# Performance work log

Measured on AMD Instinct MI355X. Metric: run time of the kernel, lower is better.

Reference implementation:

```python
import jax, jax.numpy as jnp
import numpy as np

B, S, H = 1, 2048, 2048
NH = 16
Q_LORA, KV_LORA = 1536, 512
D_NOPE, D_ROPE, D_V = 128, 64, 128
D_QK = D_NOPE + D_ROPE  # 192
EPS = 1e-6
ROPE_BASE = 10000.0


def setup_inputs() -> dict:
    key = jax.random.key(0)
    ks = jax.random.split(key, 8)
    def lin(k, fan_in, fan_out):
        # nn.Linear default init, stored as [in, out] for x @ W
        bound = 1.0 / np.sqrt(fan_in)
        return jax.random.uniform(k, (fan_in, fan_out), jnp.float32, -bound, bound)
    return {
        "hidden_states": jax.random.normal(ks[0], (B, S, H), jnp.float32),
        "Wqa": lin(ks[1], H, Q_LORA),
        "q_a_ln_w": jnp.ones((Q_LORA,), jnp.float32),
        "Wqb": lin(ks[2], Q_LORA, NH * D_QK),
        "Wkva": lin(ks[3], H, KV_LORA + D_ROPE),
        "kv_a_ln_w": jnp.ones((KV_LORA,), jnp.float32),
        "Wkvb": lin(ks[4], KV_LORA, NH * (D_NOPE + D_V)),
        "Wo": lin(ks[5], NH * D_V, H),
    }


def _rmsnorm(x, w):
    xf = x.astype(jnp.float32)
    var = jnp.mean(xf * xf, axis=-1, keepdims=True)
    return w * (xf * jax.lax.rsqrt(var + EPS)).astype(x.dtype)


def _rotate_half(x):
    x1, x2 = jnp.split(x, 2, axis=-1)
    return jnp.concatenate((-x2, x1), axis=-1)


def _rope_tables(seq_len, dtype=jnp.float32):
    inv_freq = 1.0 / (ROPE_BASE ** (jnp.arange(0, D_ROPE, 2, dtype=jnp.float32) / D_ROPE))
    t = jnp.arange(seq_len, dtype=jnp.float32)
    freqs = jnp.outer(t, inv_freq)                      # [S, D_ROPE/2]
    emb = jnp.concatenate((freqs, freqs), axis=-1)      # [S, D_ROPE]
    return jnp.cos(emb).astype(dtype), jnp.sin(emb).astype(dtype)


def reference(hidden_states, Wqa, q_a_ln_w, Wqb, Wkva, kv_a_ln_w, Wkvb, Wo):
    bsz, q_len, _ = hidden_states.shape
    scale = D_QK ** -0.5

    # Q path: LoRA down -> RMSNorm -> up
    q = _rmsnorm(hidden_states @ Wqa, q_a_ln_w) @ Wqb            # [B,S,NH*D_QK]
    q = q.reshape(bsz, q_len, NH, D_QK).transpose(0, 2, 1, 3)    # [B,NH,S,D_QK]
    q_nope, q_pe = q[..., :D_NOPE], q[..., D_NOPE:]

    # KV path: compressed latent + shared rope key
    ckv = hidden_states @ Wkva                                    # [B,S,KV_LORA+D_ROPE]
    compressed_kv, k_pe = ckv[..., :KV_LORA], ckv[..., KV_LORA:]
    k_pe = k_pe.reshape(bsz, q_len, 1, D_ROPE).transpose(0, 2, 1, 3)  # [B,1,S,D_ROPE]
    kv = _rmsnorm(compressed_kv, kv_a_ln_w) @ Wkvb                # [B,S,NH*(D_NOPE+D_V)]
    kv = kv.reshape(bsz, q_len, NH, D_NOPE + D_V).transpose(0, 2, 1, 3)
    k_nope, v = kv[..., :D_NOPE], kv[..., D_NOPE:]                # [B,NH,S,D_NOPE], [B,NH,S,D_V]

    # decoupled RoPE on the rope sub-dims
    cos, sin = _rope_tables(q_len, hidden_states.dtype)
    cos = cos[None, None]  # [1,1,S,D_ROPE] broadcast over batch & heads
    sin = sin[None, None]
    q_pe = q_pe * cos + _rotate_half(q_pe) * sin
    k_pe = k_pe * cos + _rotate_half(k_pe) * sin                  # [B,1,S,D_ROPE]

    query = jnp.concatenate([q_nope, q_pe], axis=-1)              # [B,NH,S,D_QK]
    key = jnp.concatenate([k_nope, jnp.broadcast_to(k_pe, (bsz, NH, q_len, D_ROPE))], axis=-1)

    attn = jnp.einsum('bhqd,bhkd->bhqk', query, key) * scale      # [B,NH,S,S]
    causal = jnp.triu(jnp.ones((q_len, q_len), bool), k=1)
    attn = jnp.where(causal, -jnp.inf, attn)
    attn = jax.nn.softmax(attn.astype(jnp.float32), axis=-1).astype(query.dtype)

    out = jnp.einsum('bhqk,bhkd->bhqd', attn, v)                  # [B,NH,S,D_V]
    out = out.transpose(0, 2, 1, 3).reshape(bsz, q_len, NH * D_V)
    return out @ Wo                                               # [B,S,H]
```

## Files before the change

kernel.cpp:

```cpp
#include <hip/hip_runtime.h>
#include <hip/hip_bf16.h>
#include <math.h>

#define S_LEN 2048
#define H_DIM 2048
#define NH 16
#define Q_LORA 1536
#define KV_LORA 512
#define D_NOPE 128
#define D_ROPE 64
#define D_V 128
#define D_QK 192

typedef unsigned short ushort_t;
typedef __attribute__((ext_vector_type(8))) short short8;
typedef __attribute__((ext_vector_type(4))) float f32x4;

__device__ __forceinline__ ushort_t f2bf(float f) {
    unsigned int u = __float_as_uint(f);
    u = (u + 0x7FFFu + ((u >> 16) & 1u)) >> 16;
    return (ushort_t)u;
}
__device__ __forceinline__ float bf2f(ushort_t u) {
    return __uint_as_float(((unsigned int)u) << 16);
}

__device__ __forceinline__ void storeC(float* p, float v) { *p = v; }
__device__ __forceinline__ void storeC(ushort_t* p, float v) { *p = f2bf(v); }

__device__ __forceinline__ void gload_lds16(const ushort_t* g, ushort_t* l) {
    __builtin_amdgcn_global_load_lds(
        (const __attribute__((address_space(1))) unsigned int*)(const void*)g,
        (__attribute__((address_space(3))) unsigned int*)(void*)l, 16, 0, 0);
}

__device__ __forceinline__ float dpp_max16(float x) {
    x = fmaxf(x, __int_as_float(__builtin_amdgcn_update_dpp(0, __float_as_int(x), 0xB1, 0xF, 0xF, true)));
    x = fmaxf(x, __int_as_float(__builtin_amdgcn_update_dpp(0, __float_as_int(x), 0x4E, 0xF, 0xF, true)));
    x = fmaxf(x, __int_as_float(__builtin_amdgcn_update_dpp(0, __float_as_int(x), 0x124, 0xF, 0xF, true)));
    x = fmaxf(x, __int_as_float(__builtin_amdgcn_update_dpp(0, __float_as_int(x), 0x128, 0xF, 0xF, true)));
    return x;
}
__device__ __forceinline__ float dpp_sum16(float x) {
    x += __int_as_float(__builtin_amdgcn_update_dpp(0, __float_as_int(x), 0xB1, 0xF, 0xF, true));
    x += __int_as_float(__builtin_amdgcn_update_dpp(0, __float_as_int(x), 0x4E, 0xF, 0xF, true));
    x += __int_as_float(__builtin_amdgcn_update_dpp(0, __float_as_int(x), 0x124, 0xF, 0xF, true));
    x += __int_as_float(__builtin_amdgcn_update_dpp(0, __float_as_int(x), 0x128, 0xF, 0xF, true));
    return x;
}

__device__ __forceinline__ void convT_body(
    const float* __restrict__ W, ushort_t* __restrict__ Wt,
    int K, int N, int n0, int k0, float (*tile)[33])
{
    const int tr = threadIdx.x >> 5, tc = threadIdx.x & 31;
    #pragma unroll
    for (int i = 0; i < 4; ++i) {
        int r = tr + i * 8;
        float v = 0.f;
        if (n0 + tc < N) v = W[(size_t)(k0 + r) * N + n0 + tc];
        tile[r][tc] = v;
    }
    __syncthreads();
    #pragma unroll
    for (int i = 0; i < 4; ++i) {
        int r = tr + i * 8;
        Wt[(size_t)(n0 + r) * K + k0 + tc] = f2bf(tile[tc][r]);
    }
}

__global__ __launch_bounds__(256) void unified_conv(
    const float* __restrict__ hs, ushort_t* __restrict__ hs16,
    const float* __restrict__ Wqa, const float* __restrict__ Wkva,
    const float* __restrict__ Wqb, const float* __restrict__ Wkvb,
    const float* __restrict__ Wo,
    ushort_t* __restrict__ WcatT, ushort_t* __restrict__ WqbT,
    ushort_t* __restrict__ WkvbT, ushort_t* __restrict__ WoT)
{
    __shared__ float tile[32][33];
    int b = blockIdx.x;
    if (b < 4096) {
        int base = (b * 256 + threadIdx.x) * 4;
        float4 v = *(const float4*)(hs + base);
        hs16[base + 0] = f2bf(v.x);
        hs16[base + 1] = f2bf(v.y);
        hs16[base + 2] = f2bf(v.z);
        hs16[base + 3] = f2bf(v.w);
        return;
    }
    b -= 4096;
    const float* W; ushort_t* Wt; int K, N, nbx;
    if (b < 3072)        {            W = Wqa;  Wt = WcatT;                              K = 2048; N = 1536; nbx = 48;  }
    else if (b < 4352)   { b -= 3072; W = Wkva; Wt = WcatT + (size_t)Q_LORA * H_DIM;     K = 2048; N = 576;  nbx = 20;  }
    else if (b < 8960)   { b -= 4352; W = Wqb;  Wt = WqbT;                               K = 1536; N = 3072; nbx = 96;  }
    else if (b < 11008)  { b -= 8960; W = Wkvb; Wt = WkvbT;                              K = 512;  N = 4096; nbx = 128; }
    else                 { b -= 11008; W = Wo;  Wt = WoT;                                K = 2048; N = 2048; nbx = 64;  }
    convT_body(W, Wt, K, N, (b % nbx) * 32, (b / nbx) * 32, tile);
}

__global__ __launch_bounds__(256) void fused_norm_ropek(
    const ushort_t* __restrict__ cat16r, ushort_t* __restrict__ qa16,
    ushort_t* __restrict__ ckv16n, ushort_t* __restrict__ kpe16,
    const float* __restrict__ qlnw, const float* __restrict__ klnw)
{
    __shared__ float red[4];
    const int b = blockIdx.x;
    if (b < 4096) {
        const bool isQ = (b < 2048);
        const int row = isQ ? b : b - 2048;
        const int K = isQ ? Q_LORA : KV_LORA;
        const ushort_t* x = cat16r + (size_t)row * 2176 + (isQ ? 0 : Q_LORA);
        ushort_t* y = (isQ ? qa16 + (size_t)row * Q_LORA : ckv16n + (size_t)row * KV_LORA);
        const float* wv = isQ ? qlnw : klnw;
        float ss = 0.f;
        for (int i = threadIdx.x; i < K; i += 256) { float v = bf2f(x[i]); ss += v * v; }
        #pragma unroll
        for (int off = 32; off > 0; off >>= 1) ss += __shfl_down(ss, off);
        int lane = threadIdx.x & 63, wid = threadIdx.x >> 6;
        if (lane == 0) red[wid] = ss;
        __syncthreads();
        float tot = red[0] + red[1] + red[2] + red[3];
        float rs = rsqrtf(tot / (float)K + 1e-6f);
        for (int i = threadIdx.x; i < K; i += 256)
            y[i] = f2bf(bf2f(x[i]) * rs * wv[i]);
    } else {
        int idx = (b - 4096) * 256 + threadIdx.x;
        if (idx >= S_LEN * 32) return;
        int i = idx & 31;
        int s = idx >> 5;
        float inv = powf(10000.0f, -(2.0f * i) / 64.0f);
        float ang = (float)s * inv;
        float c = cosf(ang), sn = sinf(ang);
        const ushort_t* p = cat16r + (size_t)s * 2176 + Q_LORA + KV_LORA;
        ushort_t* q = kpe16 + (size_t)s * D_ROPE;
        float x1 = bf2f(p[i]), x2 = bf2f(p[i + 32]);
        q[i]      = f2bf(x1 * c - x2 * sn);
        q[i + 32] = f2bf(x2 * c + x1 * sn);
    }
}

__global__ __launch_bounds__(256) void conv_vT_kernel(
    const ushort_t* __restrict__ kv, ushort_t* __restrict__ v16t)
{
    __shared__ ushort_t tile[32][33];
    const int h = blockIdx.z;
    const int s0 = blockIdx.x * 32, d0 = blockIdx.y * 32;
    const int tr = threadIdx.x >> 5, tc = threadIdx.x & 31;
    #pragma unroll
    for (int i = 0; i < 4; ++i) {
        int r = tr + i * 8;
        tile[r][tc] = kv[(size_t)(s0 + r) * 4096 + h * 256 + D_NOPE + d0 + tc];
    }
    __syncthreads();
    #pragma unroll
    for (int i = 0; i < 4; ++i) {
        int r = tr + i * 8;
        v16t[(size_t)h * D_V * S_LEN + (size_t)(d0 + r) * S_LEN + s0 + tc] = tile[tc][r];
    }
}

template <typename CT>
__device__ __forceinline__ void gemm_body_bk64(
    const ushort_t* __restrict__ A, const ushort_t* __restrict__ Bt,
    CT* __restrict__ C, int N, int K, int m0, int n0,
    ushort_t* Al, ushort_t* Bl)
{
    const int tid = threadIdx.x;
    const int lane = tid & 63;
    const int w = tid >> 6;
    const int lm = lane & 15, quad = lane >> 4;
    const int wr = w >> 1, wc = w & 1;

    f32x4 acc[2][4];
    #pragma unroll
    for (int a = 0; a < 2; ++a)
        #pragma unroll
        for (int b = 0; b < 4; ++b) acc[a][b] = (f32x4){0.f, 0.f, 0.f, 0.f};

    const int rrow = tid >> 2;
    const int rcol = (tid & 3) * 8;

    for (int k0 = 0; k0 < K; k0 += 64) {
        __syncthreads();
        #pragma unroll
        for (int c = 0; c < 2; ++c) {
            gload_lds16(A + (size_t)(m0 + rrow) * K + k0 + c * 32 + rcol,
                        Al + c * 2048 + tid * 8);
            #pragma unroll
            for (int i = 0; i < 2; ++i)
                gload_lds16(Bt + (size_t)(n0 + i * 64 + rrow) * K + k0 + c * 32 + rcol,
                            Bl + c * 4096 + (i * 256 + tid) * 8);
        }
        __syncthreads();

        #pragma unroll
        for (int c = 0; c < 2; ++c) {
            short8 af[2], bf[4];
            #pragma unroll
            for (int t = 0; t < 2; ++t)
                af[t] = *(const short8*)(Al + c * 2048 + (wr * 32 + t * 16 + lm) * 32 + quad * 8);
            #pragma unroll
            for (int t = 0; t < 4; ++t)
                bf[t] = *(const short8*)(Bl + c * 4096 + (wc * 64 + t * 16 + lm) * 32 + quad * 8);
            #pragma unroll
            for (int mt = 0; mt < 2; ++mt)
                #pragma unroll
                for (int nt = 0; nt < 4; ++nt)
                    acc[mt][nt] = __builtin_amdgcn_mfma_f32_16x16x32_bf16(
                        af[mt], bf[nt], acc[mt][nt], 0, 0, 0);
        }
    }

    #pragma unroll
    for (int mt = 0; mt < 2; ++mt)
        #pragma unroll
        for (int nt = 0; nt < 4; ++nt)
            #pragma unroll
            for (int r = 0; r < 4; ++r) {
                int row = m0 + wr * 32 + mt * 16 + quad * 4 + r;
                int col = n0 + wc * 64 + nt * 16 + lm;
                storeC(&C[(size_t)row * N + col], acc[mt][nt][r]);
            }
}

template <typename CT>
__global__ __launch_bounds__(256) void mfma_gemm_bt(
    const ushort_t* __restrict__ A, const ushort_t* __restrict__ Bt,
    CT* __restrict__ C, int N, int K)
{
    __shared__ ushort_t Al[2 * 64 * 32];
    __shared__ ushort_t Bl[2 * 128 * 32];
    gemm_body_bk64<CT>(A, Bt, C, N, K, blockIdx.y * 64, blockIdx.x * 128, Al, Bl);
}

__global__ __launch_bounds__(256) void mfma_gemm_dual(
    const ushort_t* __restrict__ A1, const ushort_t* __restrict__ Bt1,
    ushort_t* __restrict__ C1, int N1, int K1, int nb1,
    const ushort_t* __restrict__ A2, const ushort_t* __restrict__ Bt2,
    ushort_t* __restrict__ C2, int N2, int K2)
{
    __shared__ ushort_t Al[2 * 64 * 32];
    __shared__ ushort_t Bl[2 * 128 * 32];
    int g = blockIdx.x;
    if (g < nb1) {
        int nbx = N1 / 128;
        gemm_body_bk64<ushort_t>(A1, Bt1, C1, N1, K1, (g / nbx) * 64, (g % nbx) * 128, Al, Bl);
    } else {
        g -= nb1;
        int nbx = N2 / 128;
        gemm_body_bk64<ushort_t>(A2, Bt2, C2, N2, K2, (g / nbx) * 64, (g % nbx) * 128, Al, Bl);
    }
}

__device__ __forceinline__ void softmax_step(
    f32x4 s[4], int k0, int qw, int lm, int quad,
    float m_[4], float l_[4], f32x4 O[8], ushort_t* ps)
{
    const float scale = 0.07216878364870322f;
    #pragma unroll
    for (int r = 0; r < 4; ++r) {
        int qrow = qw + quad * 4 + r;
        float a[4];
        #pragma unroll
        for (int st = 0; st < 4; ++st)
            a[st] = (k0 + st * 16 + lm <= qrow) ? s[st][r] * scale : -1e30f;
        float mx = dpp_max16(fmaxf(fmaxf(a[0], a[1]), fmaxf(a[2], a[3])));
        float mn = fmaxf(m_[r], mx);
        float p[4];
        #pragma unroll
        for (int st = 0; st < 4; ++st) p[st] = __expf(a[st] - mn);
        float alpha = __expf(m_[r] - mn);
        float psum = dpp_sum16((p[0] + p[1]) + (p[2] + p[3]));
        l_[r] = l_[r] * alpha + psum;
        m_[r] = mn;
        #pragma unroll
        for (int c = 0; c < 8; ++c) O[c][r] *= alpha;
        #pragma unroll
        for (int st = 0; st < 4; ++st)
            ps[(quad * 4 + r) * 72 + st * 16 + lm] = f2bf(p[st]);
    }
}

__global__ __launch_bounds__(128) void mla_attn_kernel(
    const ushort_t* __restrict__ qb, const ushort_t* __restrict__ kvb,
    const ushort_t* __restrict__ kpe, const ushort_t* __restrict__ v16t,
    ushort_t* __restrict__ aout16)
{
    __shared__ ushort_t Kn[4 * 64 * 32];
    __shared__ ushort_t Kr[2 * 64 * 32];
    __shared__ ushort_t Vt[2 * 128 * 32];
    __shared__ ushort_t Ps[2][16][72];

    const int h = blockIdx.x;
    const int q0 = 32 * (63 - blockIdx.y);
    const int w = threadIdx.x >> 6;
    const int lane = threadIdx.x & 63;
    const int lm = lane & 15, quad = lane >> 4;
    const int qw = q0 + 16 * w;
    ushort_t* myPs = &Ps[w][0][0];

    short8 qf[6];
    #pragma unroll
    for (int f = 0; f < 6; ++f)
        qf[f] = *(const short8*)(qb + (size_t)(qw + lm) * 3072 + h * 192 + f * 32 + quad * 8);
    {
        float srow = (float)(qw + lm);
        #pragma unroll
        for (int j = 0; j < 8; ++j) {
            int i = quad * 8 + j;
            float inv = powf(10000.0f, -(2.0f * i) / 64.0f);
            float ang = srow * inv;
            float c = cosf(ang), sn = sinf(ang);
            float x1 = bf2f((ushort_t)qf[4][j]);
            float x2 = bf2f((ushort_t)qf[5][j]);
            qf[4][j] = (short)f2bf(x1 * c - x2 * sn);
            qf[5][j] = (short)f2bf(x2 * c + x1 * sn);
        }
    }

    f32x4 O[8];
    #pragma unroll
    for (int c = 0; c < 8; ++c) O[c] = (f32x4){0.f, 0.f, 0.f, 0.f};
    float m_[4] = {-1e30f, -1e30f, -1e30f, -1e30f};
    float l_[4] = {0.f, 0.f, 0.f, 0.f};

    const int skey = lane >> 2;
    const int ssub = (lane & 3) * 8;

    const int kend = q0 + 32;
    for (int k0 = 0; k0 < kend; k0 += 64) {
        __syncthreads();
        {
            #pragma unroll
            for (int fi = 0; fi < 2; ++fi) {
                int f = 2 * w + fi;
                #pragma unroll
                for (int i = 0; i < 4; ++i)
                    gload_lds16(kvb + (size_t)(k0 + i * 16 + skey) * 4096 + h * 256 + f * 32 + ssub,
                                Kn + f * 2048 + i * 512 + lane * 8);
            }
            #pragma unroll
            for (int i = 0; i < 4; ++i)
                gload_lds16(kpe + (size_t)(k0 + i * 16 + skey) * 64 + w * 32 + ssub,
                            Kr + w * 2048 + i * 512 + lane * 8);
            #pragma unroll
            for (int j = 0; j < 8; ++j)
                gload_lds16(v16t + ((size_t)h * 128 + j * 16 + skey) * S_LEN + k0 + w * 32 + ssub,
                            Vt + w * 4096 + j * 512 + lane * 8);
        }
        __syncthreads();

        if (k0 < qw + 16) {
            f32x4 s[4];
            #pragma unroll
            for (int st = 0; st < 4; ++st) s[st] = (f32x4){0.f, 0.f, 0.f, 0.f};
            #pragma unroll
            for (int f = 0; f < 4; ++f)
                #pragma unroll
                for (int st = 0; st < 4; ++st) {
                    short8 kf = *(const short8*)(Kn + f * 2048 + (st * 16 + lm) * 32 + quad * 8);
                    s[st] = __builtin_amdgcn_mfma_f32_16x16x32_bf16(qf[f], kf, s[st], 0, 0, 0);
                }
            #pragma unroll
            for (int f2 = 0; f2 < 2; ++f2)
                #pragma unroll
                for (int st = 0; st < 4; ++st) {
                    short8 kf = *(const short8*)(Kr + f2 * 2048 + (st * 16 + lm) * 32 + quad * 8);
                    s[st] = __builtin_amdgcn_mfma_f32_16x16x32_bf16(qf[4 + f2], kf, s[st], 0, 0, 0);
                }

            softmax_step(s, k0, qw, lm, quad, m_, l_, O, myPs);

            asm volatile("s_waitcnt lgkmcnt(0)" ::: "memory");
            short8 pf0 = *(const short8*)(myPs + lm * 72 + quad * 8);
            short8 pf1 = *(const short8*)(myPs + lm * 72 + 32 + quad * 8);
            #pragma unroll
            for (int c = 0; c < 8; ++c) {
                short8 vf0 = *(const short8*)(Vt + (c * 16 + lm) * 32 + quad * 8);
                short8 vf1 = *(const short8*)(Vt + 4096 + (c * 16 + lm) * 32 + quad * 8);
                O[c] = __builtin_amdgcn_mfma_f32_16x16x32_bf16(pf0, vf0, O[c], 0, 0, 0);
                O[c] = __builtin_amdgcn_mfma_f32_16x16x32_bf16(pf1, vf1, O[c], 0, 0, 0);
            }
        }
    }
    #pragma unroll
    for (int c = 0; c < 8; ++c)
        #pragma unroll
        for (int r = 0; r < 4; ++r) {
            int qrow = qw + quad * 4 + r;
            aout16[(size_t)qrow * 2048 + h * D_V + c * 16 + lm] = f2bf(O[c][r] / l_[r]);
        }
}

extern "C" void kernel_launch(void* const* d_in, const int* in_sizes, int n_in,
                              void* d_out, int out_size, void* d_ws, size_t ws_size,
                              hipStream_t stream)
{
    (void)in_sizes; (void)n_in; (void)out_size; (void)ws_size;
    const float* hs   = (const float*)d_in[0];
    const float* Wqa  = (const float*)d_in[1];
    const float* qlnw = (const float*)d_in[2];
    const float* Wqb  = (const float*)d_in[3];
    const float* Wkva = (const float*)d_in[4];
    const float* klnw = (const float*)d_in[5];
    const float* Wkvb = (const float*)d_in[6];
    const float* Wo   = (const float*)d_in[7];
    float* out = (float*)d_out;

    ushort_t* p = (ushort_t*)d_ws;
    ushort_t* hs16   = p; p += (size_t)S_LEN * H_DIM;
    ushort_t* WcatT  = p; p += (size_t)2176 * H_DIM;
    ushort_t* WqbT   = p; p += (size_t)3072 * Q_LORA;
    ushort_t* WkvbT  = p; p += (size_t)4096 * KV_LORA;
    ushort_t* WoT    = p; p += (size_t)H_DIM * H_DIM;
    ushort_t* cat16r = p; p += (size_t)S_LEN * 2176;
    ushort_t* qa16   = p; p += (size_t)S_LEN * Q_LORA;
    ushort_t* qbuf16 = p; p += (size_t)S_LEN * 3072;
    ushort_t* ckv16n = p; p += (size_t)S_LEN * KV_LORA;
    ushort_t* kpe16  = p; p += (size_t)S_LEN * D_ROPE;
    ushort_t* kv16   = p; p += (size_t)S_LEN * 4096;
    ushort_t* v16t   = p; p += (size_t)NH * D_V * S_LEN;
    ushort_t* aout16 = p; p += (size_t)S_LEN * 2048;

    unified_conv<<<19200, 256, 0, stream>>>(
        hs, hs16, Wqa, Wkva, Wqb, Wkvb, Wo, WcatT, WqbT, WkvbT, WoT);
    mfma_gemm_bt<ushort_t><<<dim3(2176 / 128, S_LEN / 64), 256, 0, stream>>>(
        hs16, WcatT, cat16r, 2176, H_DIM);
    fused_norm_ropek<<<4096 + 256, 256, 0, stream>>>(cat16r, qa16, ckv16n, kpe16, qlnw, klnw);
    mfma_gemm_dual<<<768 + 1024, 256, 0, stream>>>(
        qa16, WqbT, qbuf16, 3072, Q_LORA, 768,
        ckv16n, WkvbT, kv16, 4096, KV_LORA);
    conv_vT_kernel<<<dim3(S_LEN / 32, D_V / 32, NH), 256, 0, stream>>>(kv16, v16t);
    mla_attn_kernel<<<dim3(NH, 64), 128, 0, stream>>>(qbuf16, kv16, kpe16, v16t, aout16);
    mfma_gemm_bt<float><<<dim3(H_DIM / 128, S_LEN / 64), 256, 0, stream>>>(
        aout16, WoT, out, H_DIM, H_DIM);
}
```

Measured before the change: 336.8 us.

## Enlarge GEMM tiles to 128x128, swizzle attention LDS, add MFMA priority hints

```diff
diff --git a/kernel.cpp b/kernel.cpp
--- a/kernel.cpp
+++ b/kernel.cpp
@@ -160,7 +160,7 @@
 }
 
 template <typename CT>
-__device__ __forceinline__ void gemm_body_bk64(
+__device__ __forceinline__ void gemm_body_128(
     const ushort_t* __restrict__ A, const ushort_t* __restrict__ Bt,
     CT* __restrict__ C, int N, int K, int m0, int n0,
     ushort_t* Al, ushort_t* Bl)
@@ -171,9 +171,9 @@
     const int lm = lane & 15, quad = lane >> 4;
     const int wr = w >> 1, wc = w & 1;
 
-    f32x4 acc[2][4];
-    #pragma unroll
-    for (int a = 0; a < 2; ++a)
+    f32x4 acc[4][4];
+    #pragma unroll
+    for (int a = 0; a < 4; ++a)
         #pragma unroll
         for (int b = 0; b < 4; ++b) acc[a][b] = (f32x4){0.f, 0.f, 0.f, 0.f};
 
@@ -183,27 +183,27 @@
     for (int k0 = 0; k0 < K; k0 += 64) {
         __syncthreads();
         #pragma unroll
+        for (int c = 0; c < 2; ++c)
+            #pragma unroll
+            for (int half = 0; half < 2; ++half) {
+                gload_lds16(A + (size_t)(m0 + half * 64 + rrow) * K + k0 + c * 32 + rcol,
+                            Al + c * 4096 + half * 2048 + tid * 8);
+                gload_lds16(Bt + (size_t)(n0 + half * 64 + rrow) * K + k0 + c * 32 + rcol,
+                            Bl + c * 4096 + half * 2048 + tid * 8);
+            }
+        __syncthreads();
+
+        #pragma unroll
         for (int c = 0; c < 2; ++c) {
-            gload_lds16(A + (size_t)(m0 + rrow) * K + k0 + c * 32 + rcol,
-                        Al + c * 2048 + tid * 8);
-            #pragma unroll
-            for (int i = 0; i < 2; ++i)
-                gload_lds16(Bt + (size_t)(n0 + i * 64 + rrow) * K + k0 + c * 32 + rcol,
-                            Bl + c * 4096 + (i * 256 + tid) * 8);
-        }
-        __syncthreads();
-
-        #pragma unroll
-        for (int c = 0; c < 2; ++c) {
-            short8 af[2], bf[4];
-            #pragma unroll
-            for (int t = 0; t < 2; ++t)
-                af[t] = *(const short8*)(Al + c * 2048 + (wr * 32 + t * 16 + lm) * 32 + quad * 8);
+            short8 af[4], bf[4];
+            #pragma unroll
+            for (int t = 0; t < 4; ++t)
+                af[t] = *(const short8*)(Al + c * 4096 + (wr * 64 + t * 16 + lm) * 32 + quad * 8);
             #pragma unroll
             for (int t = 0; t < 4; ++t)
                 bf[t] = *(const short8*)(Bl + c * 4096 + (wc * 64 + t * 16 + lm) * 32 + quad * 8);
             #pragma unroll
-            for (int mt = 0; mt < 2; ++mt)
+            for (int mt = 0; mt < 4; ++mt)
                 #pragma unroll
                 for (int nt = 0; nt < 4; ++nt)
                     acc[mt][nt] = __builtin_amdgcn_mfma_f32_16x16x32_bf16(
@@ -212,12 +212,12 @@
     }
 
     #pragma unroll
-    for (int mt = 0; mt < 2; ++mt)
+    for (int mt = 0; mt < 4; ++mt)
         #pragma unroll
         for (int nt = 0; nt < 4; ++nt)
             #pragma unroll
             for (int r = 0; r < 4; ++r) {
-                int row = m0 + wr * 32 + mt * 16 + quad * 4 + r;
+                int row = m0 + wr * 64 + mt * 16 + quad * 4 + r;
                 int col = n0 + wc * 64 + nt * 16 + lm;
                 storeC(&C[(size_t)row * N + col], acc[mt][nt][r]);
             }
@@ -228,9 +228,9 @@
     const ushort_t* __restrict__ A, const ushort_t* __restrict__ Bt,
     CT* __restrict__ C, int N, int K)
 {
-    __shared__ ushort_t Al[2 * 64 * 32];
+    __shared__ ushort_t Al[2 * 128 * 32];
     __shared__ ushort_t Bl[2 * 128 * 32];
-    gemm_body_bk64<CT>(A, Bt, C, N, K, blockIdx.y * 64, blockIdx.x * 128, Al, Bl);
+    gemm_body_128<CT>(A, Bt, C, N, K, blockIdx.y * 128, blockIdx.x * 128, Al, Bl);
 }
 
 __global__ __launch_bounds__(256) void mfma_gemm_dual(
@@ -239,16 +239,16 @@
     const ushort_t* __restrict__ A2, const ushort_t* __restrict__ Bt2,
     ushort_t* __restrict__ C2, int N2, int K2)
 {
-    __shared__ ushort_t Al[2 * 64 * 32];
+    __shared__ ushort_t Al[2 * 128 * 32];
     __shared__ ushort_t Bl[2 * 128 * 32];
     int g = blockIdx.x;
     if (g < nb1) {
         int nbx = N1 / 128;
-        gemm_body_bk64<ushort_t>(A1, Bt1, C1, N1, K1, (g / nbx) * 64, (g % nbx) * 128, Al, Bl);
+        gemm_body_128<ushort_t>(A1, Bt1, C1, N1, K1, (g / nbx) * 128, (g % nbx) * 128, Al, Bl);
     } else {
         g -= nb1;
         int nbx = N2 / 128;
-        gemm_body_bk64<ushort_t>(A2, Bt2, C2, N2, K2, (g / nbx) * 64, (g % nbx) * 128, Al, Bl);
+        gemm_body_128<ushort_t>(A2, Bt2, C2, N2, K2, (g / nbx) * 128, (g % nbx) * 128, Al, Bl);
     }
 }
 
@@ -298,6 +298,10 @@
     const int lm = lane & 15, quad = lane >> 4;
     const int qw = q0 + 16 * w;
     ushort_t* myPs = &Ps[w][0][0];
+
+    const int skey = lane >> 2;
+    const int ssw  = ((lane & 3) ^ ((lane >> 3) & 3)) * 8;
+    const int swq  = quad ^ ((lm >> 1) & 3);
 
     short8 qf[6];
     #pragma unroll
@@ -324,9 +328,6 @@
     float m_[4] = {-1e30f, -1e30f, -1e30f, -1e30f};
     float l_[4] = {0.f, 0.f, 0.f, 0.f};
 
-    const int skey = lane >> 2;
-    const int ssub = (lane & 3) * 8;
-
     const int kend = q0 + 32;
     for (int k0 = 0; k0 < kend; k0 += 64) {
         __syncthreads();
@@ -336,16 +337,16 @@
                 int f = 2 * w + fi;
                 #pragma unroll
                 for (int i = 0; i < 4; ++i)
-                    gload_lds16(kvb + (size_t)(k0 + i * 16 + skey) * 4096 + h * 256 + f * 32 + ssub,
+                    gload_lds16(kvb + (size_t)(k0 + i * 16 + skey) * 4096 + h * 256 + f * 32 + ssw,
                                 Kn + f * 2048 + i * 512 + lane * 8);
             }
             #pragma unroll
             for (int i = 0; i < 4; ++i)
-                gload_lds16(kpe + (size_t)(k0 + i * 16 + skey) * 64 + w * 32 + ssub,
+                gload_lds16(kpe + (size_t)(k0 + i * 16 + skey) * 64 + w * 32 + ssw,
                             Kr + w * 2048 + i * 512 + lane * 8);
             #pragma unroll
             for (int j = 0; j < 8; ++j)
-                gload_lds16(v16t + ((size_t)h * 128 + j * 16 + skey) * S_LEN + k0 + w * 32 + ssub,
+                gload_lds16(v16t + ((size_t)h * 128 + j * 16 + skey) * S_LEN + k0 + w * 32 + ssw,
                             Vt + w * 4096 + j * 512 + lane * 8);
         }
         __syncthreads();
@@ -354,33 +355,37 @@
             f32x4 s[4];
             #pragma unroll
             for (int st = 0; st < 4; ++st) s[st] = (f32x4){0.f, 0.f, 0.f, 0.f};
+            __builtin_amdgcn_s_setprio(1);
             #pragma unroll
             for (int f = 0; f < 4; ++f)
                 #pragma unroll
                 for (int st = 0; st < 4; ++st) {
-                    short8 kf = *(const short8*)(Kn + f * 2048 + (st * 16 + lm) * 32 + quad * 8);
+                    short8 kf = *(const short8*)(Kn + f * 2048 + (st * 16 + lm) * 32 + swq * 8);
                     s[st] = __builtin_amdgcn_mfma_f32_16x16x32_bf16(qf[f], kf, s[st], 0, 0, 0);
                 }
             #pragma unroll
             for (int f2 = 0; f2 < 2; ++f2)
                 #pragma unroll
                 for (int st = 0; st < 4; ++st) {
-                    short8 kf = *(const short8*)(Kr + f2 * 2048 + (st * 16 + lm) * 32 + quad * 8);
+                    short8 kf = *(const short8*)(Kr + f2 * 2048 + (st * 16 + lm) * 32 + swq * 8);
                     s[st] = __builtin_amdgcn_mfma_f32_16x16x32_bf16(qf[4 + f2], kf, s[st], 0, 0, 0);
                 }
+            __builtin_amdgcn_s_setprio(0);
 
             softmax_step(s, k0, qw, lm, quad, m_, l_, O, myPs);
 
             asm volatile("s_waitcnt lgkmcnt(0)" ::: "memory");
             short8 pf0 = *(const short8*)(myPs + lm * 72 + quad * 8);
             short8 pf1 = *(const short8*)(myPs + lm * 72 + 32 + quad * 8);
+            __builtin_amdgcn_s_setprio(1);
             #pragma unroll
             for (int c = 0; c < 8; ++c) {
-                short8 vf0 = *(const short8*)(Vt + (c * 16 + lm) * 32 + quad * 8);
-                short8 vf1 = *(const short8*)(Vt + 4096 + (c * 16 + lm) * 32 + quad * 8);
+                short8 vf0 = *(const short8*)(Vt + (c * 16 + lm) * 32 + swq * 8);
+                short8 vf1 = *(const short8*)(Vt + 4096 + (c * 16 + lm) * 32 + swq * 8);
                 O[c] = __builtin_amdgcn_mfma_f32_16x16x32_bf16(pf0, vf0, O[c], 0, 0, 0);
                 O[c] = __builtin_amdgcn_mfma_f32_16x16x32_bf16(pf1, vf1, O[c], 0, 0, 0);
             }
+            __builtin_amdgcn_s_setprio(0);
         }
     }
     #pragma unroll
@@ -424,14 +429,14 @@
 
     unified_conv<<<19200, 256, 0, stream>>>(
         hs, hs16, Wqa, Wkva, Wqb, Wkvb, Wo, WcatT, WqbT, WkvbT, WoT);
-    mfma_gemm_bt<ushort_t><<<dim3(2176 / 128, S_LEN / 64), 256, 0, stream>>>(
+    mfma_gemm_bt<ushort_t><<<dim3(2176 / 128, S_LEN / 128), 256, 0, stream>>>(
         hs16, WcatT, cat16r, 2176, H_DIM);
     fused_norm_ropek<<<4096 + 256, 256, 0, stream>>>(cat16r, qa16, ckv16n, kpe16, qlnw, klnw);
-    mfma_gemm_dual<<<768 + 1024, 256, 0, stream>>>(
-        qa16, WqbT, qbuf16, 3072, Q_LORA, 768,
+    mfma_gemm_dual<<<384 + 512, 256, 0, stream>>>(
+        qa16, WqbT, qbuf16, 3072, Q_LORA, 384,
         ckv16n, WkvbT, kv16, 4096, KV_LORA);
     conv_vT_kernel<<<dim3(S_LEN / 32, D_V / 32, NH), 256, 0, stream>>>(kv16, v16t);
     mla_attn_kernel<<<dim3(NH, 64), 128, 0, stream>>>(qbuf16, kv16, kpe16, v16t, aout16);
-    mfma_gemm_bt<float><<<dim3(H_DIM / 128, S_LEN / 64), 256, 0, stream>>>(
+    mfma_gemm_bt<float><<<dim3(H_DIM / 128, S_LEN / 128), 256, 0, stream>>>(
         aout16, WoT, out, H_DIM, H_DIM);
 }
```

Result: slower. 347.5 us (+3.2%).
